# Kernel tuning notes

Hardware: AMD Instinct MI355X
Metric: run time of the kernel (lower is better)

## Reference

```python
import jax, jax.numpy as jnp
import numpy as np

B, V, N, S, F, H, K, STEPS = 8, 3, 400, 1200, 16, 32, 10, 12
ALPHA_FUSE = 0.8
NEG = -9e15


def setup_inputs() -> dict:
    key = jax.random.key(0)
    ks = jax.random.split(key, 16)
    g = lambda i, shape, s=0.1: jax.random.normal(ks[i], shape, jnp.float32) * s
    return {
        "feat": jax.random.normal(ks[0], (B, S, F), jnp.float32),
        "adj": jax.random.bernoulli(ks[1], 0.05, (B, V, S, S)).astype(jnp.float32),
        "dis_lab": jax.random.uniform(ks[2], (B, K), dtype=jnp.float32),
        "W_gat": g(3, (V, F, H), 0.3),
        "a_gat": g(4, (V, 2 * H, 1), 0.3),
        "qkv_W": g(5, (H, 3 * H)),
        "qkv_b": jnp.zeros((3 * H,), jnp.float32),
        "o_W": g(6, (H, H)),
        "o_b": jnp.zeros((H,), jnp.float32),
        "fus_W": g(7, (H, H)),
        "fus_b": jnp.zeros((H,), jnp.float32),
        "att1_W": g(8, (2 * H, H)),
        "att1_b": jnp.zeros((H,), jnp.float32),
        "att2_W": g(9, (H, 1)),
        "att2_b": jnp.zeros((1,), jnp.float32),
        "gru_Wih": g(10, (H, 3 * H)),
        "gru_Whh": g(11, (H, 3 * H)),
        "gru_bih": jnp.zeros((3 * H,), jnp.float32),
        "gru_bhh": jnp.zeros((3 * H,), jnp.float32),
        "out_W": g(12, (H, 1)),
        "out_b": jnp.zeros((1,), jnp.float32),
    }


def _forward(feat, adj, dis_lab, W_gat, a_gat, qkv_W, qkv_b, o_W, o_b,
             fus_W, fus_b, att1_W, att1_b, att2_W, att2_b,
             gru_Wih, gru_Whh, gru_bih, gru_bhh, out_W, out_b):
    # ---- per-view GAT (masked softmax over dense adjacency) ----
    Wh = jnp.einsum('bsf,vfh->bvsh', feat, W_gat)            # [B,V,S,H]
    a1, a2 = a_gat[:, :H, 0], a_gat[:, H:, 0]
    e = (jnp.einsum('bvsh,vh->bvs', Wh, a1)[..., :, None]
         + jnp.einsum('bvsh,vh->bvs', Wh, a2)[..., None, :])  # [B,V,S,S]
    e = jax.nn.leaky_relu(e, 0.2)
    e = jnp.where(adj > 0, e, NEG)
    att = jax.nn.softmax(e, axis=-1)
    hid = jax.nn.elu(jnp.einsum('bvst,bvth->bvsh', att, Wh))  # [B,V,S,H]
    # ---- cross-view self-attention fusion (single head) ----
    x = hid.reshape(B, V * S, H)
    q, k, v = jnp.split(x @ qkv_W + qkv_b, 3, axis=-1)
    logits = jnp.einsum('bld,bmd->blm', q, k) / jnp.sqrt(jnp.float32(H))
    sa = jnp.einsum('blm,bmd->bld', jax.nn.softmax(logits, axis=-1), v)
    sa = sa @ o_W + o_b
    hfuse = (ALPHA_FUSE * sa + (1.0 - ALPHA_FUSE) * x).reshape(B, V, S, H)
    gate = jax.nn.sigmoid(hfuse @ fus_W + fus_b)
    fusion = jnp.sum(gate * hfuse, axis=1)[:, 2 * N:, :]      # [B,N,H]
    # ---- attention over label stations ----
    label = fusion[:, :K, :]                                  # [B,K,H]
    unlabel = fusion[:, K, :]                                 # [B,H]
    cat = jnp.concatenate([label, jnp.broadcast_to(unlabel[:, None, :], label.shape)], axis=-1)
    s = jax.nn.relu(cat @ att1_W + att1_b) @ att2_W + att2_b  # [B,K,1]
    score = jax.nn.softmax(s[..., 0] * dis_lab, axis=1)
    ctx = jnp.einsum('bk,bkh->bh', score, label)
    # ---- GRU decoder (feed hidden state back as next input) ----
    def gru_cell(xt, h):
        gi = xt @ gru_Wih + gru_bih
        gh = h @ gru_Whh + gru_bhh
        ir, iz, inn = jnp.split(gi, 3, axis=-1)
        hr, hz, hn = jnp.split(gh, 3, axis=-1)
        r = jax.nn.sigmoid(ir + hr)
        z = jax.nn.sigmoid(iz + hz)
        n = jnp.tanh(inn + r * hn)
        return (1.0 - z) * n + z * h
    def step(carry, _):
        xt, h = carry
        h2 = gru_cell(xt, h)
        out = h2 @ out_W + out_b
        return (h2, h2), out[:, 0]
    _, outs = jax.lax.scan(step, (ctx, unlabel), None, length=STEPS)
    return outs.T  # [B, STEPS]


def reference(feat, adj, dis_lab, W_gat, a_gat, qkv_W, qkv_b, o_W, o_b,
              fus_W, fus_b, att1_W, att1_b, att2_W, att2_b,
              gru_Wih, gru_Whh, gru_bih, gru_bhh, out_W, out_b):
    return _forward(feat, adj, dis_lab, W_gat, a_gat, qkv_W, qkv_b, o_W, o_b,
                    fus_W, fus_b, att1_W, att1_b, att2_W, att2_b,
                    gru_Wih, gru_Whh, gru_bih, gru_bhh, out_W, out_b)
```

## Files before the change

kernel.cpp:

```cpp
#include <hip/hip_runtime.h>
#include <math.h>

#define Bb 8
#define Vv 3
#define Ss 1200
#define Ff 16
#define Hh 32
#define Kk 10
#define STEPS 12
#define ROWS (Bb*Vv*Ss)
#define L (Vv*Ss)
#define KPAD 1216

typedef __attribute__((ext_vector_type(8))) short bf16x8;
typedef __attribute__((ext_vector_type(4))) float f32x4;
typedef __attribute__((ext_vector_type(4))) unsigned int u32x4;

__device__ __forceinline__ unsigned int pack_hi2(float x0, float x1) {
    return (__float_as_uint(x1) & 0xFFFF0000u) | (__float_as_uint(x0) >> 16);
}
__device__ __forceinline__ unsigned int pack_lo2(float x0, float x1) {
    float h0 = __uint_as_float(__float_as_uint(x0) & 0xFFFF0000u);
    float h1 = __uint_as_float(__float_as_uint(x1) & 0xFFFF0000u);
    return (__float_as_uint(x1 - h1) & 0xFFFF0000u) | (__float_as_uint(x0 - h0) >> 16);
}

__global__ __launch_bounds__(256) void gat_wh_k(const float* __restrict__ feat,
                                                const float* __restrict__ W_gat,
                                                const float* __restrict__ a_gat,
                                                float* __restrict__ Wh,
                                                float* __restrict__ fvec,
                                                float* __restrict__ gvec) {
    int blk = blockIdx.x;
    int c = blk % 150;
    int v = (blk / 150) % Vv;
    int b = blk / (150 * Vv);
    int tid = threadIdx.x;
    int r = tid >> 5;
    int h = tid & 31;
    int s = c * 8 + r;

    __shared__ float Wg[16][32];
    __shared__ float fe[8][16];
    for (int i = tid; i < 512; i += 256) Wg[i >> 5][i & 31] = W_gat[v * 512 + i];
    for (int i = tid; i < 128; i += 256) fe[i >> 4][i & 15] = feat[(b * Ss + c * 8) * Ff + i];
    __syncthreads();

    float acc = 0.f;
#pragma unroll
    for (int k = 0; k < 16; ++k) acc += fe[r][k] * Wg[k][h];

    int row = (b * Vv + v) * Ss + s;
    Wh[(size_t)row * Hh + h] = acc;

    float a1 = a_gat[v * 64 + h];
    float a2 = a_gat[v * 64 + 32 + h];
    float pf = acc * a1, pg = acc * a2;
#pragma unroll
    for (int m = 16; m >= 1; m >>= 1) {
        pf += __shfl_xor(pf, m);
        pg += __shfl_xor(pg, m);
    }
    if (h == 0) { fvec[row] = pf; gvec[row] = pg; }
}

__global__ __launch_bounds__(256) void gmax_k(const float* __restrict__ gvec,
                                              float* __restrict__ Gmax) {
    int bv = blockIdx.x;
    int tid = threadIdx.x;
    float m = -3.0e38f;
    for (int t = tid; t < Ss; t += 256) m = fmaxf(m, gvec[bv * Ss + t]);
#pragma unroll
    for (int mm = 32; mm >= 1; mm >>= 1) m = fmaxf(m, __shfl_xor(m, mm));
    __shared__ float red[4];
    if ((tid & 63) == 0) red[tid >> 6] = m;
    __syncthreads();
    if (tid == 0) Gmax[bv] = fmaxf(fmaxf(red[0], red[1]), fmaxf(red[2], red[3]));
}

__global__ __launch_bounds__(256) void wht_k(const float* __restrict__ Wh,
                                             ushort* __restrict__ WhT_hi,
                                             ushort* __restrict__ WhT_lo) {
    int bv = blockIdx.x / 19, t = blockIdx.x % 19;
    int s0 = t * 64;
    int tid = threadIdx.x;
    __shared__ float T[64][33];
    for (int idx = tid; idx < 2048; idx += 256) {
        int r = idx >> 5, h = idx & 31;
        T[r][h] = (s0 + r < Ss) ? Wh[((size_t)bv * Ss + s0 + r) * Hh + h] : 0.f;
    }
    __syncthreads();
    int h = tid >> 3, c = tid & 7;
    unsigned int hb[4], lb[4];
#pragma unroll
    for (int j = 0; j < 4; ++j) {
        float e0 = T[c * 8 + 2 * j][h], e1 = T[c * 8 + 2 * j + 1][h];
        hb[j] = pack_hi2(e0, e1);
        lb[j] = pack_lo2(e0, e1);
    }
    size_t off = ((size_t)bv * 32 + h) * KPAD + s0 + c * 8;
    *(uint4*)(WhT_hi + off) = make_uint4(hb[0], hb[1], hb[2], hb[3]);
    *(uint4*)(WhT_lo + off) = make_uint4(lb[0], lb[1], lb[2], lb[3]);
}

__global__ __launch_bounds__(256) void gat_mfma_k(const float* __restrict__ adj,
                                                  const ushort* __restrict__ WhT_hi,
                                                  const ushort* __restrict__ WhT_lo,
                                                  const float* __restrict__ fvec,
                                                  const float* __restrict__ gvec,
                                                  const float* __restrict__ Gmax,
                                                  float* __restrict__ hid,
                                                  float* __restrict__ hsel) {
    int blk = blockIdx.x;
    int bv = blk / 75, tb = blk % 75;
    int wk = threadIdx.x >> 6, lane = threadIdx.x & 63;
    int rowbase = tb * 16;
    int lr = lane & 15, kg = lane >> 4;
    int b = bv / Vv, v = bv - b * Vv;

    int ar = rowbase + lr;
    const float* adj_r = adj + ((size_t)bv * Ss + ar) * Ss;
    const float* g_b = gvec + (size_t)bv * Ss;
    float fr = fvec[bv * Ss + ar];
    float M = fr + Gmax[bv];
    float Mr = fmaxf(M, 0.2f * M);

    f32x4 acc0 = {0.f, 0.f, 0.f, 0.f}, acc1 = {0.f, 0.f, 0.f, 0.f};
    float psum = 0.f;
    const ushort* Bh0 = WhT_hi + ((size_t)bv * 32 + lr) * KPAD;
    const ushort* Bl0 = WhT_lo + ((size_t)bv * 32 + lr) * KPAD;

    int kst = wk * 320;
    int kend = kst + 320; if (kend > KPAD) kend = KPAD;
    for (int k0 = kst; k0 < kend; k0 += 32) {
        int t0 = k0 + kg * 8;
        bf16x8 bh0 = *(const bf16x8*)(Bh0 + t0);
        bf16x8 bl0 = *(const bf16x8*)(Bl0 + t0);
        bf16x8 bh1 = *(const bf16x8*)(Bh0 + 16 * KPAD + t0);
        bf16x8 bl1 = *(const bf16x8*)(Bl0 + 16 * KPAD + t0);

        float p[8];
        if (t0 + 8 <= Ss) {
            float4 aA = *(const float4*)(adj_r + t0);
            float4 aB = *(const float4*)(adj_r + t0 + 4);
            float4 gA = *(const float4*)(g_b + t0);
            float4 gB = *(const float4*)(g_b + t0 + 4);
            float av[8] = {aA.x, aA.y, aA.z, aA.w, aB.x, aB.y, aB.z, aB.w};
            float gv[8] = {gA.x, gA.y, gA.z, gA.w, gB.x, gB.y, gB.z, gB.w};
#pragma unroll
            for (int j = 0; j < 8; ++j) {
                float e = fr + gv[j];
                e = fmaxf(e, 0.2f * e);
                float pe = __expf(e - Mr);
                p[j] = (av[j] > 0.f) ? pe : 0.f;
                psum += p[j];
            }
        } else {
#pragma unroll
            for (int j = 0; j < 8; ++j) p[j] = 0.f;
        }
        unsigned int hb[4], lb[4];
#pragma unroll
        for (int j = 0; j < 4; ++j) {
            hb[j] = pack_hi2(p[2 * j], p[2 * j + 1]);
            lb[j] = pack_lo2(p[2 * j], p[2 * j + 1]);
        }
        bf16x8 ah = __builtin_bit_cast(bf16x8, (u32x4){hb[0], hb[1], hb[2], hb[3]});
        bf16x8 al = __builtin_bit_cast(bf16x8, (u32x4){lb[0], lb[1], lb[2], lb[3]});
        acc0 = __builtin_amdgcn_mfma_f32_16x16x32_bf16(ah, bh0, acc0, 0, 0, 0);
        acc0 = __builtin_amdgcn_mfma_f32_16x16x32_bf16(ah, bl0, acc0, 0, 0, 0);
        acc0 = __builtin_amdgcn_mfma_f32_16x16x32_bf16(al, bh0, acc0, 0, 0, 0);
        acc1 = __builtin_amdgcn_mfma_f32_16x16x32_bf16(ah, bh1, acc1, 0, 0, 0);
        acc1 = __builtin_amdgcn_mfma_f32_16x16x32_bf16(ah, bl1, acc1, 0, 0, 0);
        acc1 = __builtin_amdgcn_mfma_f32_16x16x32_bf16(al, bh1, acc1, 0, 0, 0);
    }

    psum += __shfl_xor(psum, 16);
    psum += __shfl_xor(psum, 32);

    __shared__ float accS[4][2][16][17];
    __shared__ float psS[4][16];
#pragma unroll
    for (int j = 0; j < 4; ++j) {
        accS[wk][0][kg * 4 + j][lr] = acc0[j];
        accS[wk][1][kg * 4 + j][lr] = acc1[j];
    }
    if (lane < 16) psS[wk][lr] = psum;
    __syncthreads();
    if (threadIdx.x < 16)
        psS[0][threadIdx.x] += psS[1][threadIdx.x] + psS[2][threadIdx.x] + psS[3][threadIdx.x];
    __syncthreads();

    bool qb = (tb == 50);
    for (int idx = threadIdx.x; idx < 512; idx += 256) {
        int r = idx >> 5, col = idx & 31, tt = col >> 4, c = col & 15;
        float a = accS[0][tt][r][c] + accS[1][tt][r][c] + accS[2][tt][r][c] + accS[3][tt][r][c];
        float rr = a / psS[0][r];
        float hv = (rr > 0.f) ? rr : expm1f(rr);
        hid[((size_t)bv * Ss + rowbase + r) * 32 + col] = hv;
        if (qb && r < 11) hsel[(((size_t)b * Vv + v) * 11 + r) * 32 + col] = hv;
    }
}

__global__ __launch_bounds__(256) void attn_q_k(const float* __restrict__ hsel,
                                                const float* __restrict__ qkv_W,
                                                const float* __restrict__ qkv_b,
                                                float* __restrict__ qt,
                                                float* __restrict__ qc) {
    int b = blockIdx.x;
    int tid = threadIdx.x;
    __shared__ float hq[33][33];
    __shared__ float W1[32][33];
    __shared__ float W2[32][33];
    __shared__ float qS[33][33];

    for (int idx = tid; idx < 33 * 32; idx += 256) {
        int q = idx >> 5, i = idx & 31;
        int si = q / 3, v = q - si * 3;
        hq[q][i] = hsel[(((size_t)b * Vv + v) * 11 + si) * 32 + i];
    }
    for (int idx = tid; idx < 1024; idx += 256) {
        int i = idx >> 5, j = idx & 31;
        W1[i][j] = qkv_W[i * 96 + j];
        W2[i][j] = qkv_W[i * 96 + 32 + j];
    }
    __syncthreads();
    for (int idx = tid; idx < 33 * 32; idx += 256) {
        int q = idx >> 5, j = idx & 31;
        float a = qkv_b[j];
#pragma unroll
        for (int i = 0; i < 32; ++i) a += hq[q][i] * W1[i][j];
        qS[q][j] = a;
    }
    __syncthreads();
    for (int idx = tid; idx < 33 * 32; idx += 256) {
        int q = idx >> 5, i = idx & 31;
        float a = 0.f;
#pragma unroll
        for (int j = 0; j < 32; ++j) a += qS[q][j] * W2[i][j];
        qt[(size_t)b * 33 * 32 + q * 32 + i] = a;
    }
    if (tid < 33) {
        float a = 0.f;
        for (int j = 0; j < 32; ++j) a += qS[tid][j] * qkv_b[32 + j];
        qc[b * 33 + tid] = a;
    }
}

#define CH 120
#define NCH 30
#define PREC 34
__global__ __launch_bounds__(256) void attn_part_k(const float* __restrict__ hid,
                                                   const float* __restrict__ qt,
                                                   const float* __restrict__ qc,
                                                   float* __restrict__ part) {
    int blk = blockIdx.x;
    int b = blk / NCH, ch = blk % NCH;
    int k0 = ch * CH;
    int tid = threadIdx.x;
    const float inv = 0.1767766952966369f;

    __shared__ float hC[CH][33];
    __shared__ float qtS[33][33];
    __shared__ float qcS[33];
    __shared__ float lS[33][124];
    __shared__ float mS[33], lsS[33];

    for (int idx = tid; idx < CH * 32; idx += 256) {
        int r = idx >> 5, i = idx & 31;
        hC[r][i] = hid[((size_t)b * L + k0 + r) * 32 + i];
    }
    for (int idx = tid; idx < 33 * 32; idx += 256) {
        int q = idx >> 5, i = idx & 31;
        qtS[q][i] = qt[(size_t)b * 33 * 32 + q * 32 + i];
    }
    if (tid < 33) qcS[tid] = qc[b * 33 + tid];
    __syncthreads();

    for (int idx = tid; idx < 33 * CH; idx += 256) {
        int q = idx / CH, m = idx - q * CH;
        float d = 0.f;
#pragma unroll
        for (int i = 0; i < 32; ++i) d += qtS[q][i] * hC[m][i];
        lS[q][m] = (d + qcS[q]) * inv;
    }
    __syncthreads();

    int q4 = tid >> 2, j4 = tid & 3;
    if (q4 < 33) {
        float m = -3.0e38f;
        for (int k = j4; k < CH; k += 4) m = fmaxf(m, lS[q4][k]);
        m = fmaxf(m, __shfl_xor(m, 1));
        m = fmaxf(m, __shfl_xor(m, 2));
        float ssum = 0.f;
        for (int k = j4; k < CH; k += 4) {
            float p = __expf(lS[q4][k] - m);
            lS[q4][k] = p;
            ssum += p;
        }
        ssum += __shfl_xor(ssum, 1);
        ssum += __shfl_xor(ssum, 2);
        if (j4 == 0) { mS[q4] = m; lsS[q4] = ssum; }
    }
    __syncthreads();

    float* po = part + ((size_t)b * NCH + ch) * (33 * PREC);
    for (int idx = tid; idx < 33 * 32; idx += 256) {
        int q = idx >> 5, hh = idx & 31;
        float a = 0.f;
        for (int k = 0; k < CH; k += 4) {
            float4 p4 = *(const float4*)&lS[q][k];
            a += p4.x * hC[k][hh] + p4.y * hC[k+1][hh] + p4.z * hC[k+2][hh] + p4.w * hC[k+3][hh];
        }
        po[q * PREC + hh] = a;
    }
    if (tid < 33) { po[tid * PREC + 32] = mS[tid]; po[tid * PREC + 33] = lsS[tid]; }
}

__global__ __launch_bounds__(256) void attn_comb_k(const float* __restrict__ part,
                                                   const float* __restrict__ hsel,
                                                   const float* __restrict__ qkv_W,
                                                   const float* __restrict__ qkv_b,
                                                   const float* __restrict__ o_W,
                                                   const float* __restrict__ o_b,
                                                   const float* __restrict__ fus_W,
                                                   const float* __restrict__ fus_b,
                                                   float* __restrict__ hfg) {
    int b = blockIdx.x;
    int tid = threadIdx.x;
    __shared__ float RS[33][NCH];
    __shared__ float LSs[33];
    __shared__ float oS[33][33];
    __shared__ float vS[33][33];
    __shared__ float hfS[33][33];
    const float* pb = part + (size_t)b * NCH * (33 * PREC);

    if (tid < 33) {
        float M = -3.0e38f;
        for (int c = 0; c < NCH; ++c) M = fmaxf(M, pb[c * 33 * PREC + tid * PREC + 32]);
        float Lt = 0.f;
        for (int c = 0; c < NCH; ++c) {
            float w = __expf(pb[c * 33 * PREC + tid * PREC + 32] - M);
            RS[tid][c] = w;
            Lt += w * pb[c * 33 * PREC + tid * PREC + 33];
        }
        LSs[tid] = Lt;
    }
    __syncthreads();

    for (int idx = tid; idx < 33 * 32; idx += 256) {
        int q = idx >> 5, hh = idx & 31;
        float a = 0.f;
        for (int c = 0; c < NCH; ++c) a += RS[q][c] * pb[c * 33 * PREC + q * PREC + hh];
        oS[q][hh] = a / LSs[q];
    }
    __syncthreads();
    for (int idx = tid; idx < 33 * 32; idx += 256) {
        int q = idx >> 5, j = idx & 31;
        float a = qkv_b[64 + j];
#pragma unroll
        for (int i = 0; i < 32; ++i) a += oS[q][i] * qkv_W[i * 96 + 64 + j];
        vS[q][j] = a;
    }
    __syncthreads();
    for (int idx = tid; idx < 33 * 32; idx += 256) {
        int q = idx >> 5, hh = idx & 31;
        int si = q / 3, v = q - si * 3;
        float o = o_b[hh];
#pragma unroll
        for (int i = 0; i < 32; ++i) o += vS[q][i] * o_W[i * 32 + hh];
        float x = hsel[(((size_t)b * Vv + v) * 11 + si) * Hh + hh];
        hfS[q][hh] = 0.8f * o + 0.2f * x;
    }
    __syncthreads();
    for (int idx = tid; idx < 33 * 32; idx += 256) {
        int q = idx >> 5, hh = idx & 31;
        float gacc = fus_b[hh];
#pragma unroll
        for (int i = 0; i < 32; ++i) gacc += hfS[q][i] * fus_W[i * 32 + hh];
        float gate = 1.f / (1.f + __expf(-gacc));
        hfg[(size_t)(b * 33 + q) * 32 + hh] = gate * hfS[q][hh];
    }
}

__global__ __launch_bounds__(64) void head_k(const float* __restrict__ hfg,
                                             const float* __restrict__ dis_lab,
                                             const float* __restrict__ att1_W,
                                             const float* __restrict__ att1_b,
                                             const float* __restrict__ att2_W,
                                             const float* __restrict__ att2_b,
                                             const float* __restrict__ Wih,
                                             const float* __restrict__ Whh,
                                             const float* __restrict__ bih,
                                             const float* __restrict__ bhh,
                                             const float* __restrict__ out_W,
                                             const float* __restrict__ out_b,
                                             float* __restrict__ out) {
    int b = blockIdx.x;
    int tid = threadIdx.x;
    int j = tid & 31, half = tid >> 5;

    __shared__ float lab[11][32];
    __shared__ float a1T[32][68];
    __shared__ float WihT[3][32][36];
    __shared__ float WhhT[3][32][36];
    __shared__ float sc[12];
    __shared__ float xS[32], hS[32];

    for (int i = tid; i < 352; i += 64) {
        int k = i >> 5, hh = i & 31;
        float val = 0.f;
#pragma unroll
        for (int v = 0; v < 3; ++v) val += hfg[(size_t)(b * 33 + k * 3 + v) * 32 + hh];
        lab[k][hh] = val;
    }
    for (int idx = tid; idx < 2048; idx += 64) {
        int i = idx >> 5, jj = idx & 31;
        a1T[jj][i] = att1_W[idx];
    }
    for (int idx = tid; idx < 3072; idx += 64) {
        int i = idx / 96, col = idx - i * 96;
        int g = col >> 5, jj = col & 31;
        WihT[g][jj][i] = Wih[idx];
        WhhT[g][jj][i] = Whh[idx];
    }
    __syncthreads();

    float a2w = att2_W[j];
    float a1b = att1_b[j];
    float a2b = att2_b[0];
#pragma unroll
    for (int kk = 0; kk < 5; ++kk) {
        int k = 2 * kk + half;
        float t1 = a1b;
#pragma unroll
        for (int c = 0; c < 8; ++c) {
            float4 lb4 = *(const float4*)&lab[k][c * 4];
            float4 w4  = *(const float4*)&a1T[j][c * 4];
            t1 += lb4.x * w4.x + lb4.y * w4.y + lb4.z * w4.z + lb4.w * w4.w;
        }
#pragma unroll
        for (int c = 0; c < 8; ++c) {
            float4 lb4 = *(const float4*)&lab[10][c * 4];
            float4 w4  = *(const float4*)&a1T[j][32 + c * 4];
            t1 += lb4.x * w4.x + lb4.y * w4.y + lb4.z * w4.z + lb4.w * w4.w;
        }
        float val = fmaxf(t1, 0.f) * a2w;
#pragma unroll
        for (int mm = 16; mm >= 1; mm >>= 1) val += __shfl_xor(val, mm);
        if (j == 0) sc[k] = (val + a2b) * dis_lab[b * Kk + k];
    }
    __syncthreads();
    if (tid == 0) {
        float mx = sc[0];
        for (int k = 1; k < 10; ++k) mx = fmaxf(mx, sc[k]);
        float sm = 0.f;
        for (int k = 0; k < 10; ++k) { sc[k] = __expf(sc[k] - mx); sm += sc[k]; }
        for (int k = 0; k < 10; ++k) sc[k] /= sm;
    }
    __syncthreads();
    if (tid < 32) {
        float c = 0.f;
        for (int k = 0; k < 10; ++k) c += sc[k] * lab[k][tid];
        xS[tid] = c;
        hS[tid] = lab[10][tid];
    }
    __syncthreads();

    float b_ir = bih[j], b_iz = bih[32 + j], b_in = bih[64 + j];
    float b_hr = bhh[j], b_hz = bhh[32 + j], b_hn = bhh[64 + j];
    float ow = out_W[j], ob = out_b[0];
    int i0 = half * 16;

    for (int t = 0; t < STEPS; ++t) {
        float gi_r = 0.f, gi_z = 0.f, gi_n = 0.f;
        float gh_r = 0.f, gh_z = 0.f, gh_n = 0.f;
#pragma unroll
        for (int c = 0; c < 4; ++c) {
            float4 x4 = *(const float4*)&xS[i0 + c * 4];
            float4 h4 = *(const float4*)&hS[i0 + c * 4];
            float4 wr = *(const float4*)&WihT[0][j][i0 + c * 4];
            float4 wz = *(const float4*)&WihT[1][j][i0 + c * 4];
            float4 wn = *(const float4*)&WihT[2][j][i0 + c * 4];
            float4 ur = *(const float4*)&WhhT[0][j][i0 + c * 4];
            float4 uz = *(const float4*)&WhhT[1][j][i0 + c * 4];
            float4 un = *(const float4*)&WhhT[2][j][i0 + c * 4];
            gi_r += x4.x * wr.x + x4.y * wr.y + x4.z * wr.z + x4.w * wr.w;
            gi_z += x4.x * wz.x + x4.y * wz.y + x4.z * wz.z + x4.w * wz.w;
            gi_n += x4.x * wn.x + x4.y * wn.y + x4.z * wn.z + x4.w * wn.w;
            gh_r += h4.x * ur.x + h4.y * ur.y + h4.z * ur.z + h4.w * ur.w;
            gh_z += h4.x * uz.x + h4.y * uz.y + h4.z * uz.z + h4.w * uz.w;
            gh_n += h4.x * un.x + h4.y * un.y + h4.z * un.z + h4.w * un.w;
        }
        gi_r += __shfl_xor(gi_r, 32); gi_z += __shfl_xor(gi_z, 32); gi_n += __shfl_xor(gi_n, 32);
        gh_r += __shfl_xor(gh_r, 32); gh_z += __shfl_xor(gh_z, 32); gh_n += __shfl_xor(gh_n, 32);

        float hprev = hS[j];
        float r = 1.f / (1.f + __expf(-(gi_r + b_ir + gh_r + b_hr)));
        float z = 1.f / (1.f + __expf(-(gi_z + b_iz + gh_z + b_hz)));
        float n = tanhf(gi_n + b_in + r * (gh_n + b_hn));
        float hnew = (1.f - z) * n + z * hprev;

        float outp = hnew * ow;
#pragma unroll
        for (int mm = 16; mm >= 1; mm >>= 1) outp += __shfl_xor(outp, mm);
        if (tid == 0) out[b * STEPS + t] = outp + ob;
        __syncthreads();
        if (tid < 32) { hS[tid] = hnew; xS[tid] = hnew; }
        __syncthreads();
    }
}

extern "C" void kernel_launch(void* const* d_in, const int* in_sizes, int n_in,
                              void* d_out, int out_size, void* d_ws, size_t ws_size,
                              hipStream_t stream) {
    const float* feat    = (const float*)d_in[0];
    const float* adj     = (const float*)d_in[1];
    const float* dis_lab = (const float*)d_in[2];
    const float* W_gat   = (const float*)d_in[3];
    const float* a_gat   = (const float*)d_in[4];
    const float* qkv_W   = (const float*)d_in[5];
    const float* qkv_b   = (const float*)d_in[6];
    const float* o_W     = (const float*)d_in[7];
    const float* o_b     = (const float*)d_in[8];
    const float* fus_W   = (const float*)d_in[9];
    const float* fus_b   = (const float*)d_in[10];
    const float* att1_W  = (const float*)d_in[11];
    const float* att1_b  = (const float*)d_in[12];
    const float* att2_W  = (const float*)d_in[13];
    const float* att2_b  = (const float*)d_in[14];
    const float* Wih     = (const float*)d_in[15];
    const float* Whh     = (const float*)d_in[16];
    const float* bih     = (const float*)d_in[17];
    const float* bhh     = (const float*)d_in[18];
    const float* out_W   = (const float*)d_in[19];
    const float* out_b   = (const float*)d_in[20];
    float* out = (float*)d_out;

    float* ws = (float*)d_ws;
    float*  Wh     = ws;
    float*  hid    = ws;
    float*  fvec   = ws + 921600;
    float*  gvec   = ws + 950400;
    float*  Gmax   = ws + 979200;
    ushort* WhT_hi = (ushort*)(ws + 979232);
    float*  part   = ws + 979232;
    ushort* WhT_lo = (ushort*)(ws + 1446176);
    float*  hsel   = ws + 1913120;
    float*  hfg    = ws + 1921568;
    float*  qt     = ws + 1930016;
    float*  qc     = ws + 1938464;

    gat_wh_k<<<dim3(Bb * Vv * 150), dim3(256), 0, stream>>>(feat, W_gat, a_gat, Wh, fvec, gvec);
    gmax_k<<<dim3(Bb * Vv), dim3(256), 0, stream>>>(gvec, Gmax);
    wht_k<<<dim3(Bb * Vv * 19), dim3(256), 0, stream>>>(Wh, WhT_hi, WhT_lo);
    gat_mfma_k<<<dim3(Bb * Vv * 75), dim3(256), 0, stream>>>(adj, WhT_hi, WhT_lo,
                                                             fvec, gvec, Gmax, hid, hsel);
    attn_q_k<<<dim3(Bb), dim3(256), 0, stream>>>(hsel, qkv_W, qkv_b, qt, qc);
    attn_part_k<<<dim3(Bb * NCH), dim3(256), 0, stream>>>(hid, qt, qc, part);
    attn_comb_k<<<dim3(Bb), dim3(256), 0, stream>>>(part, hsel, qkv_W, qkv_b,
                                                    o_W, o_b, fus_W, fus_b, hfg);
    head_k<<<dim3(Bb), dim3(64), 0, stream>>>(hfg, dis_lab, att1_W, att1_b, att2_W, att2_b,
                                              Wih, Whh, bih, bhh, out_W, out_b, out);
}
```

Measured before the change: 139.0 us.

## Stage adjacency tiles into LDS with async double-buffered global_load_lds

The GAT kernel now loads the block's 16 adjacency rows in 256-column chunks straight into a double-buffered shared-memory tile using global_load_lds. The load of the next chunk is issued while the waves compute the current one. The K dimension per wave changes from one contiguous 320-wide range to interleaved 64-wide slices per chunk. The aim is coalesced adjacency reads, replacing per-lane strided row loads, and overlap of memory with MFMA work. In exchange it adds a barrier per chunk and extra LDS use, which may reduce occupancy.

New measurement: 143.6 us. 1.03x slower.

```diff
diff --git a/kernel.cpp b/kernel.cpp
--- a/kernel.cpp
+++ b/kernel.cpp
@@ -118,8 +118,12 @@
     int lr = lane & 15, kg = lane >> 4;
     int b = bv / Vv, v = bv - b * Vv;
 
+    __shared__ float adjS[2][16][260];
+    __shared__ float accS[4][2][16][17];
+    __shared__ float psS[4][16];
+
     int ar = rowbase + lr;
-    const float* adj_r = adj + ((size_t)bv * Ss + ar) * Ss;
+    const float* adj_blk = adj + ((size_t)bv * Ss + rowbase) * Ss;
     const float* g_b = gvec + (size_t)bv * Ss;
     float fr = fvec[bv * Ss + ar];
     float M = fr + Gmax[bv];
@@ -130,56 +134,88 @@
     const ushort* Bh0 = WhT_hi + ((size_t)bv * 32 + lr) * KPAD;
     const ushort* Bl0 = WhT_lo + ((size_t)bv * 32 + lr) * KPAD;
 
-    int kst = wk * 320;
-    int kend = kst + 320; if (kend > KPAD) kend = KPAD;
-    for (int k0 = kst; k0 < kend; k0 += 32) {
-        int t0 = k0 + kg * 8;
-        bf16x8 bh0 = *(const bf16x8*)(Bh0 + t0);
-        bf16x8 bl0 = *(const bf16x8*)(Bl0 + t0);
-        bf16x8 bh1 = *(const bf16x8*)(Bh0 + 16 * KPAD + t0);
-        bf16x8 bl1 = *(const bf16x8*)(Bl0 + 16 * KPAD + t0);
-
-        float p[8];
-        if (t0 + 8 <= Ss) {
-            float4 aA = *(const float4*)(adj_r + t0);
-            float4 aB = *(const float4*)(adj_r + t0 + 4);
-            float4 gA = *(const float4*)(g_b + t0);
-            float4 gB = *(const float4*)(g_b + t0 + 4);
-            float av[8] = {aA.x, aA.y, aA.z, aA.w, aB.x, aB.y, aB.z, aB.w};
-            float gv[8] = {gA.x, gA.y, gA.z, gA.w, gB.x, gB.y, gB.z, gB.w};
-#pragma unroll
-            for (int j = 0; j < 8; ++j) {
-                float e = fr + gv[j];
-                e = fmaxf(e, 0.2f * e);
-                float pe = __expf(e - Mr);
-                p[j] = (av[j] > 0.f) ? pe : 0.f;
-                psum += p[j];
+#define STAGE(buf, c)                                                                  \
+    {   int valid = ((c) == 4) ? 44 : 64;                \
+        _Pragma("unroll")                                                              \
+        for (int i = 0; i < 4; ++i) {                                                  \
+            int r = wk * 4 + i;                                                        \
+            const float* src = adj_blk + (size_t)r * Ss + (c) * 256 + lane * 4;        \
+            if (lane < valid)                                                          \
+                __builtin_amdgcn_global_load_lds(                                      \
+                    (const __attribute__((address_space(1))) unsigned int*)src,        \
+                    (__attribute__((address_space(3))) unsigned int*)&adjS[buf][r][0], \
+                    16, 0, 0);                                                         \
+        }                                                                              \
+    }
+
+#define STEP32(buf, koff, kglob)                                                       \
+    {   float4 Aa = *(const float4*)&adjS[buf][lr][(koff) + kg * 8];                   \
+        float4 Ab = *(const float4*)&adjS[buf][lr][(koff) + kg * 8 + 4];               \
+        int t0 = (kglob) + kg * 8;                                                     \
+        float4 Ga, Gb;                                                                 \
+        if (t0 + 8 <= Ss) {                                                            \
+            Ga = *(const float4*)(g_b + t0);                                           \
+            Gb = *(const float4*)(g_b + t0 + 4);                                       \
+        } else {                                                                       \
+            Ga = make_float4(0.f, 0.f, 0.f, 0.f);                                      \
+            Gb = Ga;                                                                   \
+        }                                                                              \
+        float av[8] = {Aa.x, Aa.y, Aa.z, Aa.w, Ab.x, Ab.y, Ab.z, Ab.w};                \
+        float gw[8] = {Ga.x, Ga.y, Ga.z, Ga.w, Gb.x, Gb.y, Gb.z, Gb.w};                \
+        float p[8];                                                                    \
+        _Pragma("unroll")                                                              \
+        for (int j = 0; j < 8; ++j) {                                                  \
+            float e = fr + gw[j];                                                      \
+            e = fmaxf(e, 0.2f * e);                                                    \
+            float pe = __expf(e - Mr);                                                 \
+            p[j] = (av[j] > 0.f) ? pe : 0.f;                                           \
+            psum += p[j];                                                              \
+        }                                                                              \
+        unsigned int hbp[4], lbp[4];                                                   \
+        _Pragma("unroll")                                                              \
+        for (int j = 0; j < 4; ++j) {                                                  \
+            hbp[j] = pack_hi2(p[2 * j], p[2 * j + 1]);                                 \
+            lbp[j] = pack_lo2(p[2 * j], p[2 * j + 1]);                                 \
+        }                                                                              \
+        bf16x8 ah = __builtin_bit_cast(bf16x8, (u32x4){hbp[0], hbp[1], hbp[2], hbp[3]}); \
+        bf16x8 al = __builtin_bit_cast(bf16x8, (u32x4){lbp[0], lbp[1], lbp[2], lbp[3]}); \
+        bf16x8 bh0 = *(const bf16x8*)(Bh0 + t0);                                       \
+        bf16x8 bl0 = *(const bf16x8*)(Bl0 + t0);                                       \
+        bf16x8 bh1 = *(const bf16x8*)(Bh0 + 16 * KPAD + t0);                           \
+        bf16x8 bl1 = *(const bf16x8*)(Bl0 + 16 * KPAD + t0);                           \
+        acc0 = __builtin_amdgcn_mfma_f32_16x16x32_bf16(ah, bh0, acc0, 0, 0, 0);        \
+        acc0 = __builtin_amdgcn_mfma_f32_16x16x32_bf16(ah, bl0, acc0, 0, 0, 0);        \
+        acc0 = __builtin_amdgcn_mfma_f32_16x16x32_bf16(al, bh0, acc0, 0, 0, 0);        \
+        acc1 = __builtin_amdgcn_mfma_f32_16x16x32_bf16(ah, bh1, acc1, 0, 0, 0);        \
+        acc1 = __builtin_amdgcn_mfma_f32_16x16x32_bf16(ah, bl1, acc1, 0, 0, 0);        \
+        acc1 = __builtin_amdgcn_mfma_f32_16x16x32_bf16(al, bh1, acc1, 0, 0, 0);        \
+    }
+
+    STAGE(0, 0);
+    __syncthreads();
+
+    for (int c = 0; c < 5; ++c) {
+        int cur = c & 1, nxt = (c + 1) & 1;
+        if (c + 1 < 5) {
+            STAGE(nxt, c + 1);
+            if (c + 1 == 4) {
+                int r = threadIdx.x >> 4, f = 176 + (threadIdx.x & 15);
+                adjS[nxt][r][f] = 0.f;
             }
-        } else {
-#pragma unroll
-            for (int j = 0; j < 8; ++j) p[j] = 0.f;
-        }
-        unsigned int hb[4], lb[4];
-#pragma unroll
-        for (int j = 0; j < 4; ++j) {
-            hb[j] = pack_hi2(p[2 * j], p[2 * j + 1]);
-            lb[j] = pack_lo2(p[2 * j], p[2 * j + 1]);
-        }
-        bf16x8 ah = __builtin_bit_cast(bf16x8, (u32x4){hb[0], hb[1], hb[2], hb[3]});
-        bf16x8 al = __builtin_bit_cast(bf16x8, (u32x4){lb[0], lb[1], lb[2], lb[3]});
-        acc0 = __builtin_amdgcn_mfma_f32_16x16x32_bf16(ah, bh0, acc0, 0, 0, 0);
-        acc0 = __builtin_amdgcn_mfma_f32_16x16x32_bf16(ah, bl0, acc0, 0, 0, 0);
-        acc0 = __builtin_amdgcn_mfma_f32_16x16x32_bf16(al, bh0, acc0, 0, 0, 0);
-        acc1 = __builtin_amdgcn_mfma_f32_16x16x32_bf16(ah, bh1, acc1, 0, 0, 0);
-        acc1 = __builtin_amdgcn_mfma_f32_16x16x32_bf16(ah, bl1, acc1, 0, 0, 0);
-        acc1 = __builtin_amdgcn_mfma_f32_16x16x32_bf16(al, bh1, acc1, 0, 0, 0);
-    }
+        }
+        int kw = wk * 64;
+        if (c < 4 || wk < 3) {
+            STEP32(cur, kw,      c * 256 + kw);
+            STEP32(cur, kw + 32, c * 256 + kw + 32);
+        }
+        __syncthreads();
+    }
+#undef STAGE
+#undef STEP32
 
     psum += __shfl_xor(psum, 16);
     psum += __shfl_xor(psum, 32);
 
-    __shared__ float accS[4][2][16][17];
-    __shared__ float psS[4][16];
 #pragma unroll
     for (int j = 0; j < 4; ++j) {
         accS[wk][0][kg * 4 + j][lr] = acc0[j];
```

## Pack dense adjacency into bitmasks before the GAT MFMA kernel

Applied to the files above, without the earlier changes.

Adds a kernel that reads the float adjacency once with wide coalesced loads and uses wave ballots to pack it into per-row 32-bit bitmasks laid out to match the MFMA lane/K-group order. The GAT MFMA kernel then loads ten mask words per lane up front and fully unrolls the K loop instead of streaming float adjacency inside it. This takes the strided per-row adjacency reads out of the MFMA inner loop. In exchange it adds a separate launch that still reads all of adj, plus a small mask buffer in the workspace.

After: 152.9 us. 10.0% more time.

```diff
diff --git a/kernel.cpp b/kernel.cpp
--- a/kernel.cpp
+++ b/kernel.cpp
@@ -11,6 +11,7 @@
 #define ROWS (Bb*Vv*Ss)
 #define L (Vv*Ss)
 #define KPAD 1216
+#define MROW 40
 
 typedef __attribute__((ext_vector_type(8))) short bf16x8;
 typedef __attribute__((ext_vector_type(4))) float f32x4;
@@ -23,6 +24,12 @@
     float h0 = __uint_as_float(__float_as_uint(x0) & 0xFFFF0000u);
     float h1 = __uint_as_float(__float_as_uint(x1) & 0xFFFF0000u);
     return (__float_as_uint(x1 - h1) & 0xFFFF0000u) | (__float_as_uint(x0 - h0) >> 16);
+}
+__device__ __forceinline__ unsigned int spread4(unsigned int x) {
+    x = (x | (x << 12)) & 0x000F000Fu;
+    x = (x | (x << 6))  & 0x03030303u;
+    x = (x | (x << 3))  & 0x11111111u;
+    return x;
 }
 
 __global__ __launch_bounds__(256) void gat_wh_k(const float* __restrict__ feat,
@@ -103,7 +110,38 @@
     *(uint4*)(WhT_lo + off) = make_uint4(lb[0], lb[1], lb[2], lb[3]);
 }
 
-__global__ __launch_bounds__(256) void gat_mfma_k(const float* __restrict__ adj,
+__global__ __launch_bounds__(256) void adj_pack_k(const float* __restrict__ adj,
+                                                  unsigned int* __restrict__ maskb) {
+    int gw = (blockIdx.x * 256 + threadIdx.x) >> 6;
+    int lane = threadIdx.x & 63;
+    for (int row = gw; row < ROWS; row += 5760) {
+        const float* ar = adj + (size_t)row * Ss;
+        unsigned int* mrow = maskb + (size_t)row * MROW;
+#pragma unroll
+        for (int c = 0; c < 5; ++c) {
+            int base = c * 256 + lane * 4;
+            bool v = (base + 3) < Ss;
+            float4 a = v ? *(const float4*)(ar + base) : make_float4(0.f, 0.f, 0.f, 0.f);
+            unsigned long long b0 = __ballot(v && (a.x > 0.f));
+            unsigned long long b1 = __ballot(v && (a.y > 0.f));
+            unsigned long long b2 = __ballot(v && (a.z > 0.f));
+            unsigned long long b3 = __ballot(v && (a.w > 0.f));
+            int nw = (c == 4) ? 6 : 8;
+            if (lane < nw) {
+                int sh = 8 * lane;
+                unsigned int B0 = (unsigned int)(b0 >> sh) & 0xFFu;
+                unsigned int B1 = (unsigned int)(b1 >> sh) & 0xFFu;
+                unsigned int B2 = (unsigned int)(b2 >> sh) & 0xFFu;
+                unsigned int B3 = (unsigned int)(b3 >> sh) & 0xFFu;
+                mrow[c * 8 + lane] = spread4(B0) | (spread4(B1) << 1)
+                                   | (spread4(B2) << 2) | (spread4(B3) << 3);
+            }
+        }
+        if (lane < 2) mrow[38 + lane] = 0u;
+    }
+}
+
+__global__ __launch_bounds__(256) void gat_mfma_k(const unsigned int* __restrict__ maskb,
                                                   const ushort* __restrict__ WhT_hi,
                                                   const ushort* __restrict__ WhT_lo,
                                                   const float* __restrict__ fvec,
@@ -119,60 +157,71 @@
     int b = bv / Vv, v = bv - b * Vv;
 
     int ar = rowbase + lr;
-    const float* adj_r = adj + ((size_t)bv * Ss + ar) * Ss;
     const float* g_b = gvec + (size_t)bv * Ss;
     float fr = fvec[bv * Ss + ar];
     float M = fr + Gmax[bv];
     float Mr = fmaxf(M, 0.2f * M);
 
+    const unsigned int* mrow = maskb + (size_t)(bv * Ss + ar) * MROW + wk * 10;
+    unsigned int mw[10];
+#pragma unroll
+    for (int i = 0; i < 5; ++i) {
+        uint2 t = *(const uint2*)(mrow + 2 * i);
+        mw[2 * i] = t.x; mw[2 * i + 1] = t.y;
+    }
+
     f32x4 acc0 = {0.f, 0.f, 0.f, 0.f}, acc1 = {0.f, 0.f, 0.f, 0.f};
     float psum = 0.f;
     const ushort* Bh0 = WhT_hi + ((size_t)bv * 32 + lr) * KPAD;
     const ushort* Bl0 = WhT_lo + ((size_t)bv * 32 + lr) * KPAD;
 
     int kst = wk * 320;
-    int kend = kst + 320; if (kend > KPAD) kend = KPAD;
-    for (int k0 = kst; k0 < kend; k0 += 32) {
-        int t0 = k0 + kg * 8;
-        bf16x8 bh0 = *(const bf16x8*)(Bh0 + t0);
-        bf16x8 bl0 = *(const bf16x8*)(Bl0 + t0);
-        bf16x8 bh1 = *(const bf16x8*)(Bh0 + 16 * KPAD + t0);
-        bf16x8 bl1 = *(const bf16x8*)(Bl0 + 16 * KPAD + t0);
-
-        float p[8];
-        if (t0 + 8 <= Ss) {
-            float4 aA = *(const float4*)(adj_r + t0);
-            float4 aB = *(const float4*)(adj_r + t0 + 4);
-            float4 gA = *(const float4*)(g_b + t0);
-            float4 gB = *(const float4*)(g_b + t0 + 4);
-            float av[8] = {aA.x, aA.y, aA.z, aA.w, aB.x, aB.y, aB.z, aB.w};
-            float gv[8] = {gA.x, gA.y, gA.z, gA.w, gB.x, gB.y, gB.z, gB.w};
+#pragma unroll
+    for (int s = 0; s < 10; ++s) {
+        int k0 = kst + s * 32;
+        if (k0 < KPAD) {
+            int t0 = k0 + kg * 8;
+            unsigned int mb = (mw[s] >> (kg * 8)) & 0xFFu;
+
+            bf16x8 bh0 = *(const bf16x8*)(Bh0 + t0);
+            bf16x8 bl0 = *(const bf16x8*)(Bl0 + t0);
+            bf16x8 bh1 = *(const bf16x8*)(Bh0 + 16 * KPAD + t0);
+            bf16x8 bl1 = *(const bf16x8*)(Bl0 + 16 * KPAD + t0);
+
+            float gv8[8];
+            if (t0 + 8 <= Ss) {
+                float4 gA = *(const float4*)(g_b + t0);
+                float4 gB = *(const float4*)(g_b + t0 + 4);
+                gv8[0] = gA.x; gv8[1] = gA.y; gv8[2] = gA.z; gv8[3] = gA.w;
+                gv8[4] = gB.x; gv8[5] = gB.y; gv8[6] = gB.z; gv8[7] = gB.w;
+            } else {
+#pragma unroll
+                for (int j = 0; j < 8; ++j) gv8[j] = 0.f;
+            }
+            float p[8];
 #pragma unroll
             for (int j = 0; j < 8; ++j) {
-                float e = fr + gv[j];
+                float e = fr + gv8[j];
                 e = fmaxf(e, 0.2f * e);
                 float pe = __expf(e - Mr);
-                p[j] = (av[j] > 0.f) ? pe : 0.f;
+                p[j] = ((mb >> j) & 1u) ? pe : 0.f;
                 psum += p[j];
             }
-        } else {
-#pragma unroll
-            for (int j = 0; j < 8; ++j) p[j] = 0.f;
-        }
-        unsigned int hb[4], lb[4];
-#pragma unroll
-        for (int j = 0; j < 4; ++j) {
-            hb[j] = pack_hi2(p[2 * j], p[2 * j + 1]);
-            lb[j] = pack_lo2(p[2 * j], p[2 * j + 1]);
-        }
-        bf16x8 ah = __builtin_bit_cast(bf16x8, (u32x4){hb[0], hb[1], hb[2], hb[3]});
-        bf16x8 al = __builtin_bit_cast(bf16x8, (u32x4){lb[0], lb[1], lb[2], lb[3]});
-        acc0 = __builtin_amdgcn_mfma_f32_16x16x32_bf16(ah, bh0, acc0, 0, 0, 0);
-        acc0 = __builtin_amdgcn_mfma_f32_16x16x32_bf16(ah, bl0, acc0, 0, 0, 0);
-        acc0 = __builtin_amdgcn_mfma_f32_16x16x32_bf16(al, bh0, acc0, 0, 0, 0);
-        acc1 = __builtin_amdgcn_mfma_f32_16x16x32_bf16(ah, bh1, acc1, 0, 0, 0);
-        acc1 = __builtin_amdgcn_mfma_f32_16x16x32_bf16(ah, bl1, acc1, 0, 0, 0);
-        acc1 = __builtin_amdgcn_mfma_f32_16x16x32_bf16(al, bh1, acc1, 0, 0, 0);
+            unsigned int hbp[4], lbp[4];
+#pragma unroll
+            for (int j = 0; j < 4; ++j) {
+                hbp[j] = pack_hi2(p[2 * j], p[2 * j + 1]);
+                lbp[j] = pack_lo2(p[2 * j], p[2 * j + 1]);
+            }
+            bf16x8 ah = __builtin_bit_cast(bf16x8, (u32x4){hbp[0], hbp[1], hbp[2], hbp[3]});
+            bf16x8 al = __builtin_bit_cast(bf16x8, (u32x4){lbp[0], lbp[1], lbp[2], lbp[3]});
+            acc0 = __builtin_amdgcn_mfma_f32_16x16x32_bf16(ah, bh0, acc0, 0, 0, 0);
+            acc0 = __builtin_amdgcn_mfma_f32_16x16x32_bf16(ah, bl0, acc0, 0, 0, 0);
+            acc0 = __builtin_amdgcn_mfma_f32_16x16x32_bf16(al, bh0, acc0, 0, 0, 0);
+            acc1 = __builtin_amdgcn_mfma_f32_16x16x32_bf16(ah, bh1, acc1, 0, 0, 0);
+            acc1 = __builtin_amdgcn_mfma_f32_16x16x32_bf16(ah, bl1, acc1, 0, 0, 0);
+            acc1 = __builtin_amdgcn_mfma_f32_16x16x32_bf16(al, bh1, acc1, 0, 0, 0);
+        }
     }
 
     psum += __shfl_xor(psum, 16);
@@ -550,11 +599,13 @@
     float*  hfg    = ws + 1921568;
     float*  qt     = ws + 1930016;
     float*  qc     = ws + 1938464;
-
+    unsigned int* maskb = (unsigned int*)(ws + 1938752);
+
+    adj_pack_k<<<dim3(1440), dim3(256), 0, stream>>>(adj, maskb);
     gat_wh_k<<<dim3(Bb * Vv * 150), dim3(256), 0, stream>>>(feat, W_gat, a_gat, Wh, fvec, gvec);
     gmax_k<<<dim3(Bb * Vv), dim3(256), 0, stream>>>(gvec, Gmax);
     wht_k<<<dim3(Bb * Vv * 19), dim3(256), 0, stream>>>(Wh, WhT_hi, WhT_lo);
-    gat_mfma_k<<<dim3(Bb * Vv * 75), dim3(256), 0, stream>>>(adj, WhT_hi, WhT_lo,
+    gat_mfma_k<<<dim3(Bb * Vv * 75), dim3(256), 0, stream>>>(maskb, WhT_hi, WhT_lo,
                                                              fvec, gvec, Gmax, hid, hsel);
     attn_q_k<<<dim3(Bb), dim3(256), 0, stream>>>(hsel, qkv_W, qkv_b, qt, qc);
     attn_part_k<<<dim3(Bb * NCH), dim3(256), 0, stream>>>(hid, qt, qc, part);
```
